# Performance work log

Hardware: AMD Instinct MI355X
Metric: run time of the kernel (lower is better)

## Reference

```python
import jax, jax.numpy as jnp
import numpy as np

N, E = 100000, 1600000
F_IN, H, C = 64, 64, 40


def setup_inputs() -> dict:
    key = jax.random.key(0)
    k = jax.random.split(key, 6)
    x = jax.random.normal(k[0], (N, F_IN), jnp.float32)
    edge_index = jax.random.randint(k[1], (2, E), 0, N, jnp.int32)
    edge_weight = jax.random.uniform(k[2], (E,), jnp.float32)
    W1 = jax.random.normal(k[3], (F_IN, H), jnp.float32) / np.sqrt(F_IN)
    b1 = jnp.zeros((H,), jnp.float32)
    W2 = jax.random.normal(k[4], (H, C), jnp.float32) / np.sqrt(H)
    b2 = jnp.zeros((C,), jnp.float32)
    return {"x": x, "edge_index": edge_index, "edge_weight": edge_weight,
            "W1": W1, "b1": b1, "W2": W2, "b2": b2}


def reference(x, edge_index, edge_weight, W1, b1, W2, b2):
    # PyG GCNConv: add self-loops (weight 1), symmetric normalization
    # D^{-1/2} (A + I) D^{-1/2}, linear transform, scatter-add, bias.
    n = x.shape[0]
    src, dst = edge_index[0], edge_index[1]
    loop = jnp.arange(n, dtype=src.dtype)
    src_f = jnp.concatenate([src, loop])
    dst_f = jnp.concatenate([dst, loop])
    w_f = jnp.concatenate([edge_weight, jnp.ones((n,), edge_weight.dtype)])
    deg = jax.ops.segment_sum(w_f, dst_f, num_segments=n)
    dinv = jnp.where(deg > 0, jax.lax.rsqrt(deg), 0.0)
    norm = dinv[src_f] * w_f * dinv[dst_f]  # [E+N]

    def conv(h, W, b):
        h = h @ W                                    # [n, d_out]
        msg = h[src_f] * norm[:, None]               # gather + scale, [E+N, d_out]
        return jax.ops.segment_sum(msg, dst_f, num_segments=n) + b

    h = jax.nn.relu(conv(x, W1, b1))
    # dropout is identity in eval mode (training=False)
    h = conv(h, W2, b2)
    return jax.nn.log_softmax(h, axis=1)
```

## Files before the change

### kernel.cpp

```cpp
#include <hip/hip_runtime.h>
#include <math.h>

#define N_NODES 100000
#define N_EDGES 1600000
#define C_DIM 40
#define NGROUPS 6250

#define BSZ 256
#define NB  ((N_NODES + BSZ - 1) / BSZ)
#define EB  4096
#define NBE ((N_EDGES + EB - 1) / EB)

#define OFF_DINV 0
#define OFF_BB   100000
#define OFF_CS   100392
#define OFF_ROW  100800
#define OFF_H    200802
#define OFF_REC2 353684
#define OFF_H1P  3553684
#define OFF_H2P  6753684
#define OFF_R1P  9953684

typedef float floatx4 __attribute__((ext_vector_type(4)));
typedef short shortx8 __attribute__((ext_vector_type(8)));

__device__ inline unsigned short f2bf(float f) {
    unsigned int u = __float_as_uint(f);
    u += 0x7FFF + ((u >> 16) & 1);
    return (unsigned short)(u >> 16);
}
__device__ inline float bf2f(unsigned short h) {
    return __uint_as_float(((unsigned int)h) << 16);
}
__device__ inline float bflo(unsigned int u) { return __uint_as_float(u << 16); }
__device__ inline float bfhi(unsigned int u) { return __uint_as_float(u & 0xFFFF0000u); }

__global__ __launch_bounds__(512) void k_hist2d(const int* __restrict__ ei,
                                                int* __restrict__ H,
                                                int* __restrict__ colsum) {
    __shared__ int bins[NB];
    int t = threadIdx.x, b = blockIdx.x;
    for (int i = t; i < NB; i += 512) bins[i] = 0;
    __syncthreads();
    int base = b * EB;
    for (int i = t; i < EB; i += 512) {
        int e = base + i;
        if (e < N_EDGES) atomicAdd(&bins[ei[N_EDGES + e] >> 8], 1);
    }
    __syncthreads();
    for (int i = t; i < NB; i += 512) {
        int c = bins[i];
        H[b * NB + i] = c;
        if (c) atomicAdd(&colsum[i], c);
    }
}

__global__ __launch_bounds__(512) void k_colscan(int* __restrict__ H,
                                                 const int* __restrict__ colsum,
                                                 int* __restrict__ bucketBase,
                                                 int* __restrict__ rowStart) {
    __shared__ int sd[512];
    __shared__ int sbase;
    int t = threadIdx.x, j = blockIdx.x;
    int p = 0;
    for (int i = t; i < j; i += 512) p += colsum[i];
    sd[t] = p;
    __syncthreads();
    for (int off = 256; off > 0; off >>= 1) {
        if (t < off) sd[t] += sd[t + off];
        __syncthreads();
    }
    if (t == 0) sbase = sd[0];
    __syncthreads();
    int base = sbase;
    if (t == 0) {
        bucketBase[j] = base;
        if (j == NB - 1) { bucketBase[NB] = base + colsum[j]; rowStart[N_NODES] = N_EDGES; }
    }
    __syncthreads();
    int val = (t < NBE) ? H[t * NB + j] : 0;
    sd[t] = val;
    __syncthreads();
    for (int off = 1; off < 512; off <<= 1) {
        int v = (t >= off) ? sd[t - off] : 0;
        __syncthreads();
        sd[t] += v;
        __syncthreads();
    }
    if (t < NBE) H[t * NB + j] = base + sd[t] - val;
}

__global__ __launch_bounds__(512) void k_scatter(const int* __restrict__ ei,
                                                 const float* __restrict__ w,
                                                 const int* __restrict__ blockBase,
                                                 int2* __restrict__ rec) {
    __shared__ int bases[NB];
    __shared__ int cur[NB];
    int t = threadIdx.x, b = blockIdx.x;
    for (int i = t; i < NB; i += 512) { bases[i] = blockBase[b * NB + i]; cur[i] = 0; }
    __syncthreads();
    int base = b * EB;
    for (int i = t; i < EB; i += 512) {
        int e = base + i;
        if (e < N_EDGES) {
            int s = ei[e], d = ei[N_EDGES + e];
            float wv = w[e];
            int bin = d >> 8;
            int pos = bases[bin] + atomicAdd(&cur[bin], 1);
            rec[pos] = make_int2(s | ((d & 255) << 17), __float_as_int(wv));
        }
    }
}

__global__ __launch_bounds__(512) void k_bsort(const int* __restrict__ bucketBase,
                                               const int2* __restrict__ rec,
                                               int2* __restrict__ rec2,
                                               float* __restrict__ dinv,
                                               int* __restrict__ rowStart) {
    __shared__ int   cnt[256];
    __shared__ float wsum[256];
    __shared__ int   cur[256];
    __shared__ int   sd[512];
    int t = threadIdx.x, b = blockIdx.x;
    if (t < 256) { cnt[t] = 0; wsum[t] = 0.f; }
    __syncthreads();
    int r0 = bucketBase[b], r1 = bucketBase[b + 1];
    for (int i = r0 + t; i < r1; i += 512) {
        int2 rv = rec[i];
        int l = (rv.x >> 17) & 255;
        atomicAdd(&cnt[l], 1);
        atomicAdd(&wsum[l], __int_as_float(rv.y));
    }
    __syncthreads();
    int val = (t < 256) ? cnt[t] : 0;
    sd[t] = val;
    __syncthreads();
    for (int off = 1; off < 512; off <<= 1) {
        int v = (t >= off) ? sd[t - off] : 0;
        __syncthreads();
        sd[t] += v;
        __syncthreads();
    }
    float dloc = 0.f;
    if (t < 256) {
        int excl = sd[t] - val;
        cur[t] = excl;
        int node = b * BSZ + t;
        dloc = rsqrtf(1.f + wsum[t]);
        if (node < N_NODES) {
            rowStart[node] = r0 + excl;
            dinv[node] = dloc;
        }
    }
    __syncthreads();
    if (t < 256) wsum[t] = dloc;
    __syncthreads();
    for (int i = r0 + t; i < r1; i += 512) {
        int2 rv = rec[i];
        int l = (rv.x >> 17) & 255;
        float cpart = __int_as_float(rv.y) * wsum[l];
        int pos = r0 + atomicAdd(&cur[l], 1);
        rec2[pos] = make_int2((rv.x & 0x1FFFF) << 7, __float_as_int(cpart));
    }
}

__global__ __launch_bounds__(256) void k_mm1(const float* __restrict__ x,
                                             const float* __restrict__ W1,
                                             const float* __restrict__ dinv,
                                             unsigned short* __restrict__ h1p) {
    int t = threadIdx.x, lane = t & 63, wv = t >> 6;
    int m = lane & 15, quad = lane >> 4;
    int wid = blockIdx.x * 4 + wv, nw = gridDim.x * 4;
    shortx8 B[2][4];
#pragma unroll
    for (int kc = 0; kc < 2; ++kc)
#pragma unroll
        for (int tt = 0; tt < 4; ++tt)
#pragma unroll
            for (int j = 0; j < 8; ++j) {
                int k = kc * 32 + quad * 8 + j;
                B[kc][tt][j] = (short)f2bf(W1[k * 64 + tt * 16 + m]);
            }
    for (int g = wid; g < NGROUPS; g += nw) {
        int n0 = g * 16;
        const float* xr = x + (long)(n0 + m) * 64 + quad * 8;
        floatx4 xa = ((const floatx4*)xr)[0];
        floatx4 xb = ((const floatx4*)(xr + 4))[0];
        floatx4 xc = ((const floatx4*)(xr + 32))[0];
        floatx4 xd = ((const floatx4*)(xr + 36))[0];
        shortx8 A0, A1;
#pragma unroll
        for (int j = 0; j < 4; ++j) {
            A0[j] = (short)f2bf(xa[j]);
            A0[4 + j] = (short)f2bf(xb[j]);
            A1[j] = (short)f2bf(xc[j]);
            A1[4 + j] = (short)f2bf(xd[j]);
        }
        floatx4 acc[4];
#pragma unroll
        for (int tt = 0; tt < 4; ++tt) {
            acc[tt] = (floatx4){0.f, 0.f, 0.f, 0.f};
            acc[tt] = __builtin_amdgcn_mfma_f32_16x16x32_bf16(A0, B[0][tt], acc[tt], 0, 0, 0);
            acc[tt] = __builtin_amdgcn_mfma_f32_16x16x32_bf16(A1, B[1][tt], acc[tt], 0, 0, 0);
        }
        floatx4 dv = ((const floatx4*)(dinv + n0 + quad * 4))[0];
#pragma unroll
        for (int reg = 0; reg < 4; ++reg) {
            int node = n0 + quad * 4 + reg;
            float d = dv[reg];
#pragma unroll
            for (int tt = 0; tt < 4; ++tt)
                h1p[(long)node * 64 + tt * 16 + m] = f2bf(acc[tt][reg] * d);
        }
    }
}

__global__ __launch_bounds__(256) void k_agg1(const int* __restrict__ rowStart,
                                              const int2* __restrict__ rec2,
                                              const float* __restrict__ dinv,
                                              const unsigned short* __restrict__ h1p,
                                              const float* __restrict__ b1,
                                              unsigned short* __restrict__ r1p) {
    __shared__ int2 cache[4][64];
    int t = threadIdx.x, lane = t & 63, wv = t >> 6;
    int node = blockIdx.x * 4 + wv;
    if (node >= N_NODES) return;
    int2* wc = cache[wv];
    wc[lane] = make_int2(0, 0);
    const char* hb = (const char*)h1p;
    int eslot = lane >> 3;
    int c = lane & 7;
    int lo = c << 4;
    float dn = dinv[node];
    float a0 = 0, a1 = 0, a2 = 0, a3 = 0, a4 = 0, a5 = 0, a6 = 0, a7 = 0;
    float g0 = 0, g1 = 0, g2 = 0, g3 = 0, g4 = 0, g5 = 0, g6 = 0, g7 = 0;
    if (eslot == 0) {
        uint4 u = *(const uint4*)(hb + ((long)node << 7) + lo);
        a0 = bflo(u.x) * dn; a1 = bfhi(u.x) * dn;
        a2 = bflo(u.y) * dn; a3 = bfhi(u.y) * dn;
        a4 = bflo(u.z) * dn; a5 = bfhi(u.z) * dn;
        a6 = bflo(u.w) * dn; a7 = bfhi(u.w) * dn;
    }
    int s0 = rowStart[node], s1 = rowStart[node + 1];
    for (int base = s0; base < s1; base += 64) {
        int idx = base + lane;
        if (idx < s1) wc[lane] = rec2[idx];
        __builtin_amdgcn_wave_barrier();
        int cnt = min(64, s1 - base);
        int j = 0;
        for (; j + 15 < cnt; j += 16) {
            int2 eA = wc[j + eslot];
            int2 eB = wc[j + 8 + eslot];
            uint4 uA = *(const uint4*)(hb + eA.x + lo);
            uint4 uB = *(const uint4*)(hb + eB.x + lo);
            float cA = __int_as_float(eA.y), cB = __int_as_float(eB.y);
            a0 = fmaf(bflo(uA.x), cA, a0); a1 = fmaf(bfhi(uA.x), cA, a1);
            a2 = fmaf(bflo(uA.y), cA, a2); a3 = fmaf(bfhi(uA.y), cA, a3);
            a4 = fmaf(bflo(uA.z), cA, a4); a5 = fmaf(bfhi(uA.z), cA, a5);
            a6 = fmaf(bflo(uA.w), cA, a6); a7 = fmaf(bfhi(uA.w), cA, a7);
            g0 = fmaf(bflo(uB.x), cB, g0); g1 = fmaf(bfhi(uB.x), cB, g1);
            g2 = fmaf(bflo(uB.y), cB, g2); g3 = fmaf(bfhi(uB.y), cB, g3);
            g4 = fmaf(bflo(uB.z), cB, g4); g5 = fmaf(bfhi(uB.z), cB, g5);
            g6 = fmaf(bflo(uB.w), cB, g6); g7 = fmaf(bfhi(uB.w), cB, g7);
        }
        for (; j < cnt; j += 8) {
            int jj = j + eslot;
            bool valid = jj < cnt;
            int2 e = wc[valid ? jj : j];
            float cc = valid ? __int_as_float(e.y) : 0.f;
            uint4 u = *(const uint4*)(hb + e.x + lo);
            a0 = fmaf(bflo(u.x), cc, a0); a1 = fmaf(bfhi(u.x), cc, a1);
            a2 = fmaf(bflo(u.y), cc, a2); a3 = fmaf(bfhi(u.y), cc, a3);
            a4 = fmaf(bflo(u.z), cc, a4); a5 = fmaf(bfhi(u.z), cc, a5);
            a6 = fmaf(bflo(u.w), cc, a6); a7 = fmaf(bfhi(u.w), cc, a7);
        }
        __builtin_amdgcn_wave_barrier();
    }
    a0 += g0; a1 += g1; a2 += g2; a3 += g3;
    a4 += g4; a5 += g5; a6 += g6; a7 += g7;
#define RED(v) v += __shfl_xor(v, 8, 64); v += __shfl_xor(v, 16, 64); v += __shfl_xor(v, 32, 64)
    RED(a0); RED(a1); RED(a2); RED(a3); RED(a4); RED(a5); RED(a6); RED(a7);
#undef RED
    if (eslot == 0) {
        floatx4 bva = ((const floatx4*)(b1 + (c << 3)))[0];
        floatx4 bvb = ((const floatx4*)(b1 + (c << 3) + 4))[0];
        shortx8 v;
        v[0] = (short)f2bf(fmaxf(a0 + bva[0], 0.f));
        v[1] = (short)f2bf(fmaxf(a1 + bva[1], 0.f));
        v[2] = (short)f2bf(fmaxf(a2 + bva[2], 0.f));
        v[3] = (short)f2bf(fmaxf(a3 + bva[3], 0.f));
        v[4] = (short)f2bf(fmaxf(a4 + bvb[0], 0.f));
        v[5] = (short)f2bf(fmaxf(a5 + bvb[1], 0.f));
        v[6] = (short)f2bf(fmaxf(a6 + bvb[2], 0.f));
        v[7] = (short)f2bf(fmaxf(a7 + bvb[3], 0.f));
        *(shortx8*)(r1p + ((long)node << 6) + (c << 3)) = v;
    }
}

__global__ __launch_bounds__(256) void k_mm2(const unsigned short* __restrict__ r1p,
                                             const float* __restrict__ W2,
                                             const float* __restrict__ dinv,
                                             unsigned short* __restrict__ h2p) {
    int t = threadIdx.x, lane = t & 63, wv = t >> 6;
    int m = lane & 15, quad = lane >> 4;
    int wid = blockIdx.x * 4 + wv, nw = gridDim.x * 4;
    shortx8 B[2][3];
#pragma unroll
    for (int kc = 0; kc < 2; ++kc)
#pragma unroll
        for (int tt = 0; tt < 3; ++tt) {
            int n = tt * 16 + m;
#pragma unroll
            for (int j = 0; j < 8; ++j) {
                int k = kc * 32 + quad * 8 + j;
                B[kc][tt][j] = (n < C_DIM) ? (short)f2bf(W2[k * C_DIM + n]) : (short)0;
            }
        }
    for (int g = wid; g < NGROUPS; g += nw) {
        int n0 = g * 16;
        const unsigned short* rr = r1p + ((long)(n0 + m) << 6) + quad * 8;
        shortx8 A0 = *(const shortx8*)rr;
        shortx8 A1 = *(const shortx8*)(rr + 32);
        floatx4 acc[3];
#pragma unroll
        for (int tt = 0; tt < 3; ++tt) {
            acc[tt] = (floatx4){0.f, 0.f, 0.f, 0.f};
            acc[tt] = __builtin_amdgcn_mfma_f32_16x16x32_bf16(A0, B[0][tt], acc[tt], 0, 0, 0);
            acc[tt] = __builtin_amdgcn_mfma_f32_16x16x32_bf16(A1, B[1][tt], acc[tt], 0, 0, 0);
        }
        floatx4 dv = ((const floatx4*)(dinv + n0 + quad * 4))[0];
#pragma unroll
        for (int reg = 0; reg < 4; ++reg) {
            int node = n0 + quad * 4 + reg;
            float d = dv[reg];
#pragma unroll
            for (int tt = 0; tt < 3; ++tt) {
                int col = tt * 16 + m;
                if (col < C_DIM)
                    h2p[((long)node << 6) + col] = f2bf(acc[tt][reg] * d);
            }
        }
    }
}

__global__ __launch_bounds__(256) void k_agg2(const int* __restrict__ rowStart,
                                              const int2* __restrict__ rec2,
                                              const float* __restrict__ dinv,
                                              const unsigned short* __restrict__ h2p,
                                              const float* __restrict__ b2,
                                              float* __restrict__ out) {
    __shared__ int2 cache[4][64];
    int t = threadIdx.x, lane = t & 63, wv = t >> 6;
    int node = blockIdx.x * 4 + wv;
    if (node >= N_NODES) return;
    int2* wc = cache[wv];
    wc[lane] = make_int2(0, 0);
    const char* hb = (const char*)h2p;
    int eslot = lane / 10;
    int c = lane - eslot * 10;
    bool elane = eslot < 6;
    int lo = c << 3;
    float dn = dinv[node];
    float a0 = 0, a1 = 0, a2 = 0, a3 = 0;
    float g0 = 0, g1 = 0, g2 = 0, g3 = 0;
    if (eslot == 0) {
        uint2 u = *(const uint2*)(hb + ((long)node << 7) + lo);
        a0 = bflo(u.x) * dn; a1 = bfhi(u.x) * dn;
        a2 = bflo(u.y) * dn; a3 = bfhi(u.y) * dn;
    }
    int s0 = rowStart[node], s1 = rowStart[node + 1];
    for (int base = s0; base < s1; base += 64) {
        int idx = base + lane;
        if (idx < s1) wc[lane] = rec2[idx];
        __builtin_amdgcn_wave_barrier();
        int cnt = min(64, s1 - base);
        int j = 0;
        for (; j + 11 < cnt; j += 12) {
            int2 eA = wc[j + eslot];
            int2 eB = wc[j + 6 + eslot];
            uint2 uA = *(const uint2*)(hb + eA.x + lo);
            uint2 uB = *(const uint2*)(hb + eB.x + lo);
            float cA = elane ? __int_as_float(eA.y) : 0.f;
            float cB = elane ? __int_as_float(eB.y) : 0.f;
            a0 = fmaf(bflo(uA.x), cA, a0); a1 = fmaf(bfhi(uA.x), cA, a1);
            a2 = fmaf(bflo(uA.y), cA, a2); a3 = fmaf(bfhi(uA.y), cA, a3);
            g0 = fmaf(bflo(uB.x), cB, g0); g1 = fmaf(bfhi(uB.x), cB, g1);
            g2 = fmaf(bflo(uB.y), cB, g2); g3 = fmaf(bfhi(uB.y), cB, g3);
        }
        for (; j < cnt; j += 6) {
            int jj = j + eslot;
            bool valid = elane && (jj < cnt);
            int2 e = wc[valid ? jj : j];
            float cc = valid ? __int_as_float(e.y) : 0.f;
            uint2 u = *(const uint2*)(hb + e.x + lo);
            a0 = fmaf(bflo(u.x), cc, a0); a1 = fmaf(bfhi(u.x), cc, a1);
            a2 = fmaf(bflo(u.y), cc, a2); a3 = fmaf(bfhi(u.y), cc, a3);
        }
        __builtin_amdgcn_wave_barrier();
    }
    a0 += g0; a1 += g1; a2 += g2; a3 += g3;
#define RED6(v) v += __shfl(v, (lane + 30) & 63, 64); \
                v += __shfl(v, (lane + 10) & 63, 64) + __shfl(v, (lane + 20) & 63, 64)
    RED6(a0); RED6(a1); RED6(a2); RED6(a3);
#undef RED6
    bool act = lane < 10;
    floatx4 bb = act ? ((const floatx4*)(b2 + (c << 2)))[0] : (floatx4){0, 0, 0, 0};
    float v0 = act ? a0 + bb[0] : -INFINITY;
    float v1 = act ? a1 + bb[1] : -INFINITY;
    float v2 = act ? a2 + bb[2] : -INFINITY;
    float v3 = act ? a3 + bb[3] : -INFINITY;
    float m = fmaxf(fmaxf(v0, v1), fmaxf(v2, v3));
#pragma unroll
    for (int off = 32; off; off >>= 1) m = fmaxf(m, __shfl_xor(m, off, 64));
    float s = act ? (expf(v0 - m) + expf(v1 - m)) + (expf(v2 - m) + expf(v3 - m)) : 0.f;
#pragma unroll
    for (int off = 32; off; off >>= 1) s += __shfl_xor(s, off, 64);
    float ls = m + logf(s);
    if (act) {
        *(float4*)(out + (long)node * C_DIM + (c << 2)) =
            make_float4(v0 - ls, v1 - ls, v2 - ls, v3 - ls);
    }
}

extern "C" void kernel_launch(void* const* d_in, const int* in_sizes, int n_in,
                              void* d_out, int out_size, void* d_ws, size_t ws_size,
                              hipStream_t stream) {
    const float* x  = (const float*)d_in[0];
    const int*   ei = (const int*)d_in[1];
    const float* w  = (const float*)d_in[2];
    const float* W1 = (const float*)d_in[3];
    const float* b1 = (const float*)d_in[4];
    const float* W2 = (const float*)d_in[5];
    const float* b2 = (const float*)d_in[6];
    float* out = (float*)d_out;

    float* wsf = (float*)d_ws;
    int*   wsi = (int*)d_ws;
    float* dinv       = wsf + OFF_DINV;
    int*   bucketBase = wsi + OFF_BB;
    int*   colsum     = wsi + OFF_CS;
    int*   rowStart   = wsi + OFF_ROW;
    int*   H          = wsi + OFF_H;
    int2*  rec2       = (int2*)(wsi + OFF_REC2);
    int2*  rec        = (int2*)(wsi + OFF_H1P);
    unsigned short* h1p = (unsigned short*)(wsi + OFF_H1P);
    unsigned short* h2p = (unsigned short*)(wsi + OFF_H2P);
    unsigned short* r1p = (unsigned short*)(wsi + OFF_R1P);

    hipMemsetAsync(colsum, 0, NB * sizeof(int), stream);
    k_hist2d<<<NBE, 512, 0, stream>>>(ei, H, colsum);
    k_colscan<<<NB, 512, 0, stream>>>(H, colsum, bucketBase, rowStart);
    k_scatter<<<NBE, 512, 0, stream>>>(ei, w, H, rec);
    k_bsort<<<NB, 512, 0, stream>>>(bucketBase, rec, rec2, dinv, rowStart);

    k_mm1<<<512, 256, 0, stream>>>(x, W1, dinv, h1p);
    k_agg1<<<(N_NODES + 3) / 4, 256, 0, stream>>>(rowStart, rec2, dinv, h1p, b1, r1p);

    k_mm2<<<512, 256, 0, stream>>>(r1p, W2, dinv, h2p);
    k_agg2<<<(N_NODES + 3) / 4, 256, 0, stream>>>(rowStart, rec2, dinv, h2p, b2, out);
}
```

Baseline: 280.4 us.

## Stage scatter in shared memory and remap aggregation lanes to 16x4 layout

The scatter kernel now counting-sorts each edge block's records by bucket in shared memory before writing them out, so global writes to each bucket land contiguously instead of scattered. Both aggregation kernels switch to 16 lanes per edge with 8-byte loads and 4 edges in flight per iteration, which gives more memory-level parallelism per wave. In agg2 this replaces the awkward 10x6 lane split and its rotating-shuffle reduction with xor shuffles. The matmul grids are doubled. The costs are more shared-memory use and extra barriers in scatter, plus smaller per-lane loads in agg1.

```diff
diff --git a/kernel.cpp b/kernel.cpp
--- a/kernel.cpp
+++ b/kernel.cpp
@@ -28,9 +28,6 @@
     unsigned int u = __float_as_uint(f);
     u += 0x7FFF + ((u >> 16) & 1);
     return (unsigned short)(u >> 16);
-}
-__device__ inline float bf2f(unsigned short h) {
-    return __uint_as_float(((unsigned int)h) << 16);
 }
 __device__ inline float bflo(unsigned int u) { return __uint_as_float(u << 16); }
 __device__ inline float bfhi(unsigned int u) { return __uint_as_float(u & 0xFFFF0000u); }
@@ -94,21 +91,50 @@
                                                  const float* __restrict__ w,
                                                  const int* __restrict__ blockBase,
                                                  int2* __restrict__ rec) {
-    __shared__ int bases[NB];
-    __shared__ int cur[NB];
+    __shared__ int2 staged[EB];
+    __shared__ unsigned short sbin[EB];
+    __shared__ int lcnt[NB];
+    __shared__ int lbase[NB];
+    __shared__ int lcur[NB];
+    __shared__ int sd[512];
     int t = threadIdx.x, b = blockIdx.x;
-    for (int i = t; i < NB; i += 512) { bases[i] = blockBase[b * NB + i]; cur[i] = 0; }
-    __syncthreads();
     int base = b * EB;
-    for (int i = t; i < EB; i += 512) {
-        int e = base + i;
-        if (e < N_EDGES) {
-            int s = ei[e], d = ei[N_EDGES + e];
-            float wv = w[e];
-            int bin = d >> 8;
-            int pos = bases[bin] + atomicAdd(&cur[bin], 1);
-            rec[pos] = make_int2(s | ((d & 255) << 17), __float_as_int(wv));
-        }
+    int cnt = min(EB, N_EDGES - base);
+    for (int i = t; i < NB; i += 512) lcnt[i] = 0;
+    __syncthreads();
+    int  myBin[8];
+    int2 myRec[8];
+    int nMine = 0;
+    for (int i = t; i < cnt; i += 512) {
+        int s = ei[base + i], d = ei[N_EDGES + base + i];
+        float wv = w[base + i];
+        int bin = d >> 8;
+        myBin[nMine] = bin;
+        myRec[nMine] = make_int2(s | ((d & 255) << 17), __float_as_int(wv));
+        ++nMine;
+        atomicAdd(&lcnt[bin], 1);
+    }
+    __syncthreads();
+    int v = (t < NB) ? lcnt[t] : 0;
+    sd[t] = v;
+    __syncthreads();
+    for (int off = 1; off < 512; off <<= 1) {
+        int u = (t >= off) ? sd[t - off] : 0;
+        __syncthreads();
+        sd[t] += u;
+        __syncthreads();
+    }
+    if (t < NB) { lbase[t] = sd[t] - v; lcur[t] = sd[t] - v; }
+    __syncthreads();
+    for (int k = 0; k < nMine; ++k) {
+        int pos = atomicAdd(&lcur[myBin[k]], 1);
+        staged[pos] = myRec[k];
+        sbin[pos] = (unsigned short)myBin[k];
+    }
+    __syncthreads();
+    for (int i = t; i < cnt; i += 512) {
+        int bin = sbin[i];
+        rec[blockBase[b * NB + bin] + (i - lbase[bin])] = staged[i];
     }
 }
 
@@ -228,18 +254,16 @@
     int2* wc = cache[wv];
     wc[lane] = make_int2(0, 0);
     const char* hb = (const char*)h1p;
-    int eslot = lane >> 3;
-    int c = lane & 7;
-    int lo = c << 4;
+    int eslot = lane >> 4;
+    int c = lane & 15;
+    int lo = c << 3;
     float dn = dinv[node];
-    float a0 = 0, a1 = 0, a2 = 0, a3 = 0, a4 = 0, a5 = 0, a6 = 0, a7 = 0;
-    float g0 = 0, g1 = 0, g2 = 0, g3 = 0, g4 = 0, g5 = 0, g6 = 0, g7 = 0;
+    float a0 = 0, a1 = 0, a2 = 0, a3 = 0;
+    float g0 = 0, g1 = 0, g2 = 0, g3 = 0;
     if (eslot == 0) {
-        uint4 u = *(const uint4*)(hb + ((long)node << 7) + lo);
+        uint2 u = *(const uint2*)(hb + ((long)node << 7) + lo);
         a0 = bflo(u.x) * dn; a1 = bfhi(u.x) * dn;
         a2 = bflo(u.y) * dn; a3 = bfhi(u.y) * dn;
-        a4 = bflo(u.z) * dn; a5 = bfhi(u.z) * dn;
-        a6 = bflo(u.w) * dn; a7 = bfhi(u.w) * dn;
     }
     int s0 = rowStart[node], s1 = rowStart[node + 1];
     for (int base = s0; base < s1; base += 64) {
@@ -249,51 +273,47 @@
         int cnt = min(64, s1 - base);
         int j = 0;
         for (; j + 15 < cnt; j += 16) {
-            int2 eA = wc[j + eslot];
-            int2 eB = wc[j + 8 + eslot];
-            uint4 uA = *(const uint4*)(hb + eA.x + lo);
-            uint4 uB = *(const uint4*)(hb + eB.x + lo);
-            float cA = __int_as_float(eA.y), cB = __int_as_float(eB.y);
-            a0 = fmaf(bflo(uA.x), cA, a0); a1 = fmaf(bfhi(uA.x), cA, a1);
-            a2 = fmaf(bflo(uA.y), cA, a2); a3 = fmaf(bfhi(uA.y), cA, a3);
-            a4 = fmaf(bflo(uA.z), cA, a4); a5 = fmaf(bfhi(uA.z), cA, a5);
-            a6 = fmaf(bflo(uA.w), cA, a6); a7 = fmaf(bfhi(uA.w), cA, a7);
-            g0 = fmaf(bflo(uB.x), cB, g0); g1 = fmaf(bfhi(uB.x), cB, g1);
-            g2 = fmaf(bflo(uB.y), cB, g2); g3 = fmaf(bfhi(uB.y), cB, g3);
-            g4 = fmaf(bflo(uB.z), cB, g4); g5 = fmaf(bfhi(uB.z), cB, g5);
-            g6 = fmaf(bflo(uB.w), cB, g6); g7 = fmaf(bfhi(uB.w), cB, g7);
-        }
-        for (; j < cnt; j += 8) {
+            int2 e0 = wc[j + eslot];
+            int2 e1 = wc[j + 4 + eslot];
+            int2 e2 = wc[j + 8 + eslot];
+            int2 e3 = wc[j + 12 + eslot];
+            uint2 u0 = *(const uint2*)(hb + e0.x + lo);
+            uint2 u1 = *(const uint2*)(hb + e1.x + lo);
+            uint2 u2 = *(const uint2*)(hb + e2.x + lo);
+            uint2 u3 = *(const uint2*)(hb + e3.x + lo);
+            float c0 = __int_as_float(e0.y), c1 = __int_as_float(e1.y);
+            float c2 = __int_as_float(e2.y), c3 = __int_as_float(e3.y);
+            a0 = fmaf(bflo(u0.x), c0, a0); a1 = fmaf(bfhi(u0.x), c0, a1);
+            a2 = fmaf(bflo(u0.y), c0, a2); a3 = fmaf(bfhi(u0.y), c0, a3);
+            g0 = fmaf(bflo(u1.x), c1, g0); g1 = fmaf(bfhi(u1.x), c1, g1);
+            g2 = fmaf(bflo(u1.y), c1, g2); g3 = fmaf(bfhi(u1.y), c1, g3);
+            a0 = fmaf(bflo(u2.x), c2, a0); a1 = fmaf(bfhi(u2.x), c2, a1);
+            a2 = fmaf(bflo(u2.y), c2, a2); a3 = fmaf(bfhi(u2.y), c2, a3);
+            g0 = fmaf(bflo(u3.x), c3, g0); g1 = fmaf(bfhi(u3.x), c3, g1);
+            g2 = fmaf(bflo(u3.y), c3, g2); g3 = fmaf(bfhi(u3.y), c3, g3);
+        }
+        for (; j < cnt; j += 4) {
             int jj = j + eslot;
             bool valid = jj < cnt;
             int2 e = wc[valid ? jj : j];
             float cc = valid ? __int_as_float(e.y) : 0.f;
-            uint4 u = *(const uint4*)(hb + e.x + lo);
+            uint2 u = *(const uint2*)(hb + e.x + lo);
             a0 = fmaf(bflo(u.x), cc, a0); a1 = fmaf(bfhi(u.x), cc, a1);
             a2 = fmaf(bflo(u.y), cc, a2); a3 = fmaf(bfhi(u.y), cc, a3);
-            a4 = fmaf(bflo(u.z), cc, a4); a5 = fmaf(bfhi(u.z), cc, a5);
-            a6 = fmaf(bflo(u.w), cc, a6); a7 = fmaf(bfhi(u.w), cc, a7);
         }
         __builtin_amdgcn_wave_barrier();
     }
     a0 += g0; a1 += g1; a2 += g2; a3 += g3;
-    a4 += g4; a5 += g5; a6 += g6; a7 += g7;
-#define RED(v) v += __shfl_xor(v, 8, 64); v += __shfl_xor(v, 16, 64); v += __shfl_xor(v, 32, 64)
-    RED(a0); RED(a1); RED(a2); RED(a3); RED(a4); RED(a5); RED(a6); RED(a7);
+#define RED(v) v += __shfl_xor(v, 16, 64); v += __shfl_xor(v, 32, 64)
+    RED(a0); RED(a1); RED(a2); RED(a3);
 #undef RED
     if (eslot == 0) {
-        floatx4 bva = ((const floatx4*)(b1 + (c << 3)))[0];
-        floatx4 bvb = ((const floatx4*)(b1 + (c << 3) + 4))[0];
-        shortx8 v;
-        v[0] = (short)f2bf(fmaxf(a0 + bva[0], 0.f));
-        v[1] = (short)f2bf(fmaxf(a1 + bva[1], 0.f));
-        v[2] = (short)f2bf(fmaxf(a2 + bva[2], 0.f));
-        v[3] = (short)f2bf(fmaxf(a3 + bva[3], 0.f));
-        v[4] = (short)f2bf(fmaxf(a4 + bvb[0], 0.f));
-        v[5] = (short)f2bf(fmaxf(a5 + bvb[1], 0.f));
-        v[6] = (short)f2bf(fmaxf(a6 + bvb[2], 0.f));
-        v[7] = (short)f2bf(fmaxf(a7 + bvb[3], 0.f));
-        *(shortx8*)(r1p + ((long)node << 6) + (c << 3)) = v;
+        floatx4 bv = ((const floatx4*)(b1 + (c << 2)))[0];
+        unsigned int w0 = f2bf(fmaxf(a0 + bv[0], 0.f)) |
+                          ((unsigned int)f2bf(fmaxf(a1 + bv[1], 0.f)) << 16);
+        unsigned int w1 = f2bf(fmaxf(a2 + bv[2], 0.f)) |
+                          ((unsigned int)f2bf(fmaxf(a3 + bv[3], 0.f)) << 16);
+        *(uint2*)(r1p + ((long)node << 6) + (c << 2)) = make_uint2(w0, w1);
     }
 }
 
@@ -356,10 +376,10 @@
     int2* wc = cache[wv];
     wc[lane] = make_int2(0, 0);
     const char* hb = (const char*)h2p;
-    int eslot = lane / 10;
-    int c = lane - eslot * 10;
-    bool elane = eslot < 6;
-    int lo = c << 3;
+    int eslot = lane >> 4;
+    int c = lane & 15;
+    bool act = c < 10;
+    int lo = (act ? c : 9) << 3;
     float dn = dinv[node];
     float a0 = 0, a1 = 0, a2 = 0, a3 = 0;
     float g0 = 0, g1 = 0, g2 = 0, g3 = 0;
@@ -375,21 +395,29 @@
         __builtin_amdgcn_wave_barrier();
         int cnt = min(64, s1 - base);
         int j = 0;
-        for (; j + 11 < cnt; j += 12) {
-            int2 eA = wc[j + eslot];
-            int2 eB = wc[j + 6 + eslot];
-            uint2 uA = *(const uint2*)(hb + eA.x + lo);
-            uint2 uB = *(const uint2*)(hb + eB.x + lo);
-            float cA = elane ? __int_as_float(eA.y) : 0.f;
-            float cB = elane ? __int_as_float(eB.y) : 0.f;
-            a0 = fmaf(bflo(uA.x), cA, a0); a1 = fmaf(bfhi(uA.x), cA, a1);
-            a2 = fmaf(bflo(uA.y), cA, a2); a3 = fmaf(bfhi(uA.y), cA, a3);
-            g0 = fmaf(bflo(uB.x), cB, g0); g1 = fmaf(bfhi(uB.x), cB, g1);
-            g2 = fmaf(bflo(uB.y), cB, g2); g3 = fmaf(bfhi(uB.y), cB, g3);
-        }
-        for (; j < cnt; j += 6) {
+        for (; j + 15 < cnt; j += 16) {
+            int2 e0 = wc[j + eslot];
+            int2 e1 = wc[j + 4 + eslot];
+            int2 e2 = wc[j + 8 + eslot];
+            int2 e3 = wc[j + 12 + eslot];
+            uint2 u0 = *(const uint2*)(hb + e0.x + lo);
+            uint2 u1 = *(const uint2*)(hb + e1.x + lo);
+            uint2 u2 = *(const uint2*)(hb + e2.x + lo);
+            uint2 u3 = *(const uint2*)(hb + e3.x + lo);
+            float c0 = __int_as_float(e0.y), c1 = __int_as_float(e1.y);
+            float c2 = __int_as_float(e2.y), c3 = __int_as_float(e3.y);
+            a0 = fmaf(bflo(u0.x), c0, a0); a1 = fmaf(bfhi(u0.x), c0, a1);
+            a2 = fmaf(bflo(u0.y), c0, a2); a3 = fmaf(bfhi(u0.y), c0, a3);
+            g0 = fmaf(bflo(u1.x), c1, g0); g1 = fmaf(bfhi(u1.x), c1, g1);
+            g2 = fmaf(bflo(u1.y), c1, g2); g3 = fmaf(bfhi(u1.y), c1, g3);
+            a0 = fmaf(bflo(u2.x), c2, a0); a1 = fmaf(bfhi(u2.x), c2, a1);
+            a2 = fmaf(bflo(u2.y), c2, a2); a3 = fmaf(bfhi(u2.y), c2, a3);
+            g0 = fmaf(bflo(u3.x), c3, g0); g1 = fmaf(bfhi(u3.x), c3, g1);
+            g2 = fmaf(bflo(u3.y), c3, g2); g3 = fmaf(bfhi(u3.y), c3, g3);
+        }
+        for (; j < cnt; j += 4) {
             int jj = j + eslot;
-            bool valid = elane && (jj < cnt);
+            bool valid = jj < cnt;
             int2 e = wc[valid ? jj : j];
             float cc = valid ? __int_as_float(e.y) : 0.f;
             uint2 u = *(const uint2*)(hb + e.x + lo);
@@ -399,24 +427,26 @@
         __builtin_amdgcn_wave_barrier();
     }
     a0 += g0; a1 += g1; a2 += g2; a3 += g3;
-#define RED6(v) v += __shfl(v, (lane + 30) & 63, 64); \
-                v += __shfl(v, (lane + 10) & 63, 64) + __shfl(v, (lane + 20) & 63, 64)
-    RED6(a0); RED6(a1); RED6(a2); RED6(a3);
-#undef RED6
-    bool act = lane < 10;
+#define RED(v) v += __shfl_xor(v, 16, 64); v += __shfl_xor(v, 32, 64)
+    RED(a0); RED(a1); RED(a2); RED(a3);
+#undef RED
     floatx4 bb = act ? ((const floatx4*)(b2 + (c << 2)))[0] : (floatx4){0, 0, 0, 0};
     float v0 = act ? a0 + bb[0] : -INFINITY;
     float v1 = act ? a1 + bb[1] : -INFINITY;
     float v2 = act ? a2 + bb[2] : -INFINITY;
     float v3 = act ? a3 + bb[3] : -INFINITY;
     float m = fmaxf(fmaxf(v0, v1), fmaxf(v2, v3));
-#pragma unroll
-    for (int off = 32; off; off >>= 1) m = fmaxf(m, __shfl_xor(m, off, 64));
+    m = fmaxf(m, __shfl_xor(m, 1, 64));
+    m = fmaxf(m, __shfl_xor(m, 2, 64));
+    m = fmaxf(m, __shfl_xor(m, 4, 64));
+    m = fmaxf(m, __shfl_xor(m, 8, 64));
     float s = act ? (expf(v0 - m) + expf(v1 - m)) + (expf(v2 - m) + expf(v3 - m)) : 0.f;
-#pragma unroll
-    for (int off = 32; off; off >>= 1) s += __shfl_xor(s, off, 64);
+    s += __shfl_xor(s, 1, 64);
+    s += __shfl_xor(s, 2, 64);
+    s += __shfl_xor(s, 4, 64);
+    s += __shfl_xor(s, 8, 64);
     float ls = m + logf(s);
-    if (act) {
+    if (eslot == 0 && act) {
         *(float4*)(out + (long)node * C_DIM + (c << 2)) =
             make_float4(v0 - ls, v1 - ls, v2 - ls, v3 - ls);
     }
@@ -453,9 +483,9 @@
     k_scatter<<<NBE, 512, 0, stream>>>(ei, w, H, rec);
     k_bsort<<<NB, 512, 0, stream>>>(bucketBase, rec, rec2, dinv, rowStart);
 
-    k_mm1<<<512, 256, 0, stream>>>(x, W1, dinv, h1p);
+    k_mm1<<<1024, 256, 0, stream>>>(x, W1, dinv, h1p);
     k_agg1<<<(N_NODES + 3) / 4, 256, 0, stream>>>(rowStart, rec2, dinv, h1p, b1, r1p);
 
-    k_mm2<<<512, 256, 0, stream>>>(r1p, W2, dinv, h2p);
+    k_mm2<<<1024, 256, 0, stream>>>(r1p, W2, dinv, h2p);
     k_agg2<<<(N_NODES + 3) / 4, 256, 0, stream>>>(rowStart, rec2, dinv, h2p, b2, out);
 }
```

Result: no change. 285.8 us (+1.9%).
